# Kernel optimization log

Hardware: AMD Instinct MI355X
Metric: run time of the kernel (lower is better)

## Reference

```python
import jax, jax.numpy as jnp
import numpy as np

# DeepNovo config constants
MASS_H2O = 18.01056
MASS_NH3 = 17.02655
MS_RESOLUTION = 10.0          # bins per Dalton
WINDOW_SIZE = 10
MAX_MZ = 30000                # 3000 Da * 10 bins/Da
_PAD, _GO, _EOS = 0, 1, 2
VOCAB = 26
BATCH = 32768


def setup_inputs() -> dict:
    key = jax.random.key(0)
    k1, k2, k3, k4 = jax.random.split(key, 4)
    spectrum = jax.random.uniform(k1, (MAX_MZ,), dtype=jnp.float32)
    pepmass = jax.random.uniform(k2, (BATCH,), dtype=jnp.float32, minval=500.0, maxval=2500.0)
    prefix_mass = jax.random.uniform(k3, (BATCH,), dtype=jnp.float32) * pepmass * 0.8
    # amino-acid residue masses roughly in [57, 186] Da
    masses = jax.random.uniform(k4, (VOCAB,), dtype=jnp.float32, minval=57.0, maxval=186.0)
    return {"spectrum": spectrum, "pepmass": pepmass, "prefix_mass": prefix_mass,
            "masses": masses, "direction": 0}


def reference(spectrum, pepmass, prefix_mass, masses, direction):
    if direction == 0:
        first_label, last_label = _GO, _EOS
        cb = prefix_mass[:, None] + masses[None, :]      # [B, V]
        cy = pepmass[:, None] - cb
    else:
        first_label, last_label = _EOS, _GO
        cy = prefix_mass[:, None] + masses[None, :]
        cb = pepmass[:, None] - cy
    # 8 ion types: b, b-H2O, b-NH3, b++, y, y-H2O, y-NH3, y++  -> [B, V, 8]
    ion_mass = jnp.stack([cb, cb - MASS_H2O, cb - MASS_NH3, cb / 2,
                          cy, cy - MASS_H2O, cy - MASS_NH3, cy / 2], axis=-1)
    inf_idx = jnp.round(ion_mass * MS_RESOLUTION).astype(jnp.int32) - WINDOW_SIZE // 2
    valid = (inf_idx >= 0) & (inf_idx <= MAX_MZ - WINDOW_SIZE)   # [B, V, 8]
    safe = jnp.where(valid, inf_idx, 0)
    slices = safe[..., None] + jnp.arange(WINDOW_SIZE, dtype=jnp.int32)  # [B, V, 8, W]
    gathered = jnp.take(spectrum, slices) * valid[..., None].astype(spectrum.dtype)
    # zero out FIRST/LAST/PAD vocab rows (for both directions the set is {_PAD,_GO,_EOS})
    label_mask = jnp.ones((VOCAB,), spectrum.dtype).at[
        jnp.array([_PAD, first_label, last_label])].set(0.0)
    return gathered * label_mask[None, :, None, None]
```

## Files before the change

kernel.cpp:

```cpp
#include <hip/hip_runtime.h>
#include <hip/hip_fp16.h>


#define MASS_H2O 18.01056f
#define MASS_NH3 17.02655f

typedef float floatx4 __attribute__((ext_vector_type(4)));

constexpr int MAX_MZ = 30000;
constexpr int WIN = 10;
constexpr int CPR = 520;
constexpr int BLOCK = 960;
constexpr int GRID  = 494;
constexpr int THREADS = GRID * BLOCK;
constexpr int ROW_STEP = THREADS / CPR;
constexpr int KIT = 36;
constexpr int CHUNK = 18;
constexpr int KMAX = 37;
constexpr int DROWS = 3;
constexpr int SPAD = 30004;

__global__ __launch_bounds__(BLOCK) void intensity_kernel(
    const float* __restrict__ spectrum,
    const float* __restrict__ pepmass,
    const float* __restrict__ prefix_mass,
    const float* __restrict__ masses,
    const int*   __restrict__ dir_p,
    float* __restrict__ out,
    int batch)
{
    __shared__ __half  sspec[SPAD];
    __shared__ float2  spmf[DROWS * KMAX];

    const int tid  = (int)blockIdx.x * BLOCK + (int)threadIdx.x;
    const int blkR = ((int)blockIdx.x * BLOCK) / CPR;

    {
        const float2* sp2 = reinterpret_cast<const float2*>(spectrum);
        __half2* dst = reinterpret_cast<__half2*>(sspec);
#pragma unroll 4
        for (int i = threadIdx.x; i < MAX_MZ / 2; i += BLOCK) {
            float2 t = sp2[i];
            dst[i] = __floats2half2_rn(t.x, t.y);
        }
        if (threadIdx.x < (SPAD - MAX_MZ) / 2)
            dst[MAX_MZ / 2 + threadIdx.x] = __floats2half2_rn(0.f, 0.f);
    }
    {
        int i = threadIdx.x;
        if (i < DROWS * KMAX) {
            int d = i / KMAX;
            int k = i - d * KMAX;
            int r = blkR + d + k * ROW_STEP;
            float2 val = {0.0f, 0.0f};
            if (r < batch) { val.x = pepmass[r]; val.y = prefix_mass[r]; }
            spmf[i] = val;
        }
    }

    const int col  = tid % CPR;
    const int row0 = tid / CPR;
    const int doff = (row0 - blkR) * KMAX;
    const int v = col / 20;
    const int q = col - v * 20;
    const float ms = masses[v];
    const bool lmb = (v > 2);
    const int dir = dir_p[0];

    const int e0 = 4 * q;
    const int ionA = e0 / 10,       wp0 = e0 - ionA * 10;
    const int ionB = (e0 + 2) / 10, wp1 = (e0 + 2) - ionB * 10;
    const bool suA = ((ionA >= 4) ^ (dir != 0));
    const bool suB = ((ionB >= 4) ^ (dir != 0));
    const int  kA = ionA & 3, kB = ionB & 3;
    const float ajA = (kA == 1) ? -MASS_H2O : (kA == 2) ? -MASS_NH3 : 0.0f;
    const float ajB = (kB == 1) ? -MASS_H2O : (kB == 2) ? -MASS_NH3 : 0.0f;
    const float mjA = (kA == 3) ? 5.0f : 10.0f;
    const float mjB = (kB == 3) ? 5.0f : 10.0f;

    __syncthreads();

    const bool lastOk = (row0 + (KIT - 1) * ROW_STEP) < batch;
    floatx4* op = reinterpret_cast<floatx4*>(out) + tid;
    const uint32_t* spec32 = reinterpret_cast<const uint32_t*>(sspec);

    floatx4 vbuf[CHUNK];

    for (int ph = 0; ph < KIT / CHUNK; ++ph) {
        const int kbase = ph * CHUNK;

#pragma unroll
        for (int kk = 0; kk < CHUNK; ++kk) {
            const int k = kbase + kk;
            float2 pp = spmf[doff + k];
            float t = pp.y + ms;
            float u = pp.x - t;

            float baseA = suA ? u : t;
            float fA = (baseA + ajA) * mjA;
            int idxA = (int)rintf(fA) - (WIN / 2);
            bool vA = (unsigned)idxA <= (unsigned)(MAX_MZ - WIN);
            int safeA = vA ? idxA : 0;
            float okA = (vA && lmb) ? 1.0f : 0.0f;

            float baseB = suB ? u : t;
            float fB = (baseB + ajB) * mjB;
            int idxB = (int)rintf(fB) - (WIN / 2);
            bool vB = (unsigned)idxB <= (unsigned)(MAX_MZ - WIN);
            int safeB = vB ? idxB : 0;
            float okB = (vB && lmb) ? 1.0f : 0.0f;

            int h0 = safeA + wp0, h1 = safeB + wp1;
            int dw0 = h0 >> 1,    dw1 = h1 >> 1;
            uint32_t a0 = spec32[dw0], a1 = spec32[dw0 + 1];
            uint32_t b0 = spec32[dw1], b1 = spec32[dw1 + 1];
            uint32_t r0 = (uint32_t)(((((uint64_t)a1) << 32) | a0) >> ((h0 & 1) << 4));
            uint32_t r1 = (uint32_t)(((((uint64_t)b1) << 32) | b0) >> ((h1 & 1) << 4));
            __half2 hv0 = *reinterpret_cast<__half2*>(&r0);
            __half2 hv1 = *reinterpret_cast<__half2*>(&r1);

            floatx4 r;
            r.x = __low2float(hv0)  * okA;
            r.y = __high2float(hv0) * okA;
            r.z = __low2float(hv1)  * okB;
            r.w = __high2float(hv1) * okB;
            vbuf[kk] = r;
        }

#pragma unroll
        for (int kk = 0; kk < CHUNK; ++kk) {
            const int k = kbase + kk;
            if (k != KIT - 1 || lastOk)
                op[(size_t)k * (size_t)THREADS] = vbuf[kk];
        }
    }
}

extern "C" void kernel_launch(void* const* d_in, const int* in_sizes, int n_in,
                              void* d_out, int out_size, void* d_ws, size_t ws_size,
                              hipStream_t stream) {
    const float* spectrum    = (const float*)d_in[0];
    const float* pepmass     = (const float*)d_in[1];
    const float* prefix_mass = (const float*)d_in[2];
    const float* masses      = (const float*)d_in[3];
    const int*   direction   = (const int*)d_in[4];
    float* out = (float*)d_out;

    int batch = in_sizes[1];
    intensity_kernel<<<GRID, BLOCK, 0, stream>>>(
        spectrum, pepmass, prefix_mass, masses, direction, out, batch);
}
```

Baseline: 273.5 us.

## Assign each wave a contiguous output window with per-column flag table

Work is remapped so that each wave writes a contiguous span of output float4s, 64 lanes stepping through the span across 36 iterations, instead of each thread striding by the whole grid. Per-column constants (mass, ion selectors, window offsets, label mask) are precomputed into a shared-memory table with packed flags, and each iteration reads its column entry from that table. Block size rises to 1024, and the grid is sized from the batch, so fewer blocks each stage the spectrum into LDS. The trade is an extra LDS table read and flag decode per iteration, in exchange for more local write streams and less redundant spectrum staging.

```diff
diff --git a/kernel.cpp b/kernel.cpp
--- a/kernel.cpp
+++ b/kernel.cpp
@@ -10,15 +10,12 @@
 constexpr int MAX_MZ = 30000;
 constexpr int WIN = 10;
 constexpr int CPR = 520;
-constexpr int BLOCK = 960;
-constexpr int GRID  = 494;
-constexpr int THREADS = GRID * BLOCK;
-constexpr int ROW_STEP = THREADS / CPR;
+constexpr int BLOCK = 1024;
 constexpr int KIT = 36;
-constexpr int CHUNK = 18;
-constexpr int KMAX = 37;
-constexpr int DROWS = 3;
+constexpr int WAVE_WIN = KIT * 64;
+constexpr int BLK_WIN = (BLOCK / 64) * WAVE_WIN;
 constexpr int SPAD = 30004;
+constexpr int NROW = 73;
 
 __global__ __launch_bounds__(BLOCK) void intensity_kernel(
     const float* __restrict__ spectrum,
@@ -30,10 +27,12 @@
     int batch)
 {
     __shared__ __half  sspec[SPAD];
-    __shared__ float2  spmf[DROWS * KMAX];
+    __shared__ uint2   stbl[CPR];
+    __shared__ float2  spmf[NROW];
 
-    const int tid  = (int)blockIdx.x * BLOCK + (int)threadIdx.x;
-    const int blkR = ((int)blockIdx.x * BLOCK) / CPR;
+    const unsigned fb      = (unsigned)blockIdx.x * (unsigned)BLK_WIN;
+    const unsigned totalF  = (unsigned)batch * (unsigned)CPR;
+    const unsigned rowBase = fb / (unsigned)CPR;
 
     {
         const float2* sp2 = reinterpret_cast<const float2*>(spectrum);
@@ -46,93 +45,100 @@
         if (threadIdx.x < (SPAD - MAX_MZ) / 2)
             dst[MAX_MZ / 2 + threadIdx.x] = __floats2half2_rn(0.f, 0.f);
     }
-    {
-        int i = threadIdx.x;
-        if (i < DROWS * KMAX) {
-            int d = i / KMAX;
-            int k = i - d * KMAX;
-            int r = blkR + d + k * ROW_STEP;
-            float2 val = {0.0f, 0.0f};
-            if (r < batch) { val.x = pepmass[r]; val.y = prefix_mass[r]; }
-            spmf[i] = val;
-        }
+    if (threadIdx.x < NROW) {
+        int r = (int)rowBase + (int)threadIdx.x;
+        float2 val = {0.0f, 0.0f};
+        if (r < batch) { val.x = pepmass[r]; val.y = prefix_mass[r]; }
+        spmf[threadIdx.x] = val;
     }
-
-    const int col  = tid % CPR;
-    const int row0 = tid / CPR;
-    const int doff = (row0 - blkR) * KMAX;
-    const int v = col / 20;
-    const int q = col - v * 20;
-    const float ms = masses[v];
-    const bool lmb = (v > 2);
-    const int dir = dir_p[0];
-
-    const int e0 = 4 * q;
-    const int ionA = e0 / 10,       wp0 = e0 - ionA * 10;
-    const int ionB = (e0 + 2) / 10, wp1 = (e0 + 2) - ionB * 10;
-    const bool suA = ((ionA >= 4) ^ (dir != 0));
-    const bool suB = ((ionB >= 4) ^ (dir != 0));
-    const int  kA = ionA & 3, kB = ionB & 3;
-    const float ajA = (kA == 1) ? -MASS_H2O : (kA == 2) ? -MASS_NH3 : 0.0f;
-    const float ajB = (kB == 1) ? -MASS_H2O : (kB == 2) ? -MASS_NH3 : 0.0f;
-    const float mjA = (kA == 3) ? 5.0f : 10.0f;
-    const float mjB = (kB == 3) ? 5.0f : 10.0f;
-
+    if (threadIdx.x < CPR) {
+        const int c = threadIdx.x;
+        const int dir = dir_p[0];
+        int v = c / 20, q = c - 20 * v;
+        int e0 = 4 * q;
+        int ionA = e0 / 10,       wp0 = e0 - 10 * ionA;
+        int ionB = (e0 + 2) / 10, wp1 = (e0 + 2) - 10 * ionB;
+        int kA = ionA & 3, kB = ionB & 3;
+        unsigned fl = (unsigned)wp0 | ((unsigned)wp1 << 4);
+        if ((ionA >= 4) ^ (dir != 0)) fl |= 1u << 8;
+        if ((ionB >= 4) ^ (dir != 0)) fl |= 1u << 9;
+        if (kA == 3) fl |= 1u << 10;
+        if (kB == 3) fl |= 1u << 11;
+        if (v > 2)   fl |= 1u << 12;
+        if (kA == 1) fl |= 1u << 16;
+        if (kA == 2) fl |= 1u << 17;
+        if (kB == 1) fl |= 1u << 18;
+        if (kB == 2) fl |= 1u << 19;
+        uint2 e;
+        e.x = __float_as_uint(masses[v]);
+        e.y = fl;
+        stbl[c] = e;
+    }
     __syncthreads();
 
-    const bool lastOk = (row0 + (KIT - 1) * ROW_STEP) < batch;
-    floatx4* op = reinterpret_cast<floatx4*>(out) + tid;
+    const int wv   = (int)threadIdx.x >> 6;
+    const int lane = (int)threadIdx.x & 63;
+    unsigned f   = fb + (unsigned)wv * (unsigned)WAVE_WIN + (unsigned)lane;
+    unsigned row = f / (unsigned)CPR;
+    unsigned col = f - row * (unsigned)CPR;
+    unsigned rel = row - rowBase;
+
     const uint32_t* spec32 = reinterpret_cast<const uint32_t*>(sspec);
+    floatx4* out4 = reinterpret_cast<floatx4*>(out);
 
-    floatx4 vbuf[CHUNK];
+#pragma unroll 4
+    for (int k = 0; k < KIT; ++k) {
+        float2 pp = spmf[rel];
+        uint2  tb = stbl[col];
+        float  ms = __uint_as_float(tb.x);
+        unsigned fl = tb.y;
+        float t = pp.y + ms;
+        float u = pp.x - t;
 
-    for (int ph = 0; ph < KIT / CHUNK; ++ph) {
-        const int kbase = ph * CHUNK;
+        float baseA = (fl & (1u << 8)) ? u : t;
+        float ajA = (fl & (1u << 16)) ? -MASS_H2O
+                  : (fl & (1u << 17)) ? -MASS_NH3 : 0.0f;
+        float mjA = (fl & (1u << 10)) ? 5.0f : 10.0f;
+        float fA = (baseA + ajA) * mjA;
+        int idxA = (int)rintf(fA) - (WIN / 2);
+        bool vA = (unsigned)idxA <= (unsigned)(MAX_MZ - WIN);
+        int safeA = vA ? idxA : 0;
+        float baseB = (fl & (1u << 9)) ? u : t;
+        float ajB = (fl & (1u << 18)) ? -MASS_H2O
+                  : (fl & (1u << 19)) ? -MASS_NH3 : 0.0f;
+        float mjB = (fl & (1u << 11)) ? 5.0f : 10.0f;
+        float fB = (baseB + ajB) * mjB;
+        int idxB = (int)rintf(fB) - (WIN / 2);
+        bool vB = (unsigned)idxB <= (unsigned)(MAX_MZ - WIN);
+        int safeB = vB ? idxB : 0;
 
-#pragma unroll
-        for (int kk = 0; kk < CHUNK; ++kk) {
-            const int k = kbase + kk;
-            float2 pp = spmf[doff + k];
-            float t = pp.y + ms;
-            float u = pp.x - t;
+        bool lmb = (fl & (1u << 12)) != 0;
+        float okA = (vA && lmb) ? 1.0f : 0.0f;
+        float okB = (vB && lmb) ? 1.0f : 0.0f;
 
-            float baseA = suA ? u : t;
-            float fA = (baseA + ajA) * mjA;
-            int idxA = (int)rintf(fA) - (WIN / 2);
-            bool vA = (unsigned)idxA <= (unsigned)(MAX_MZ - WIN);
-            int safeA = vA ? idxA : 0;
-            float okA = (vA && lmb) ? 1.0f : 0.0f;
+        int h0 = safeA + (int)(fl & 15u);
+        int h1 = safeB + (int)((fl >> 4) & 15u);
+        int dw0 = h0 >> 1, dw1 = h1 >> 1;
+        uint32_t a0 = spec32[dw0], a1 = spec32[dw0 + 1];
+        uint32_t b0 = spec32[dw1], b1 = spec32[dw1 + 1];
+        uint32_t r0 = (uint32_t)(((((uint64_t)a1) << 32) | a0) >> ((h0 & 1) << 4));
+        uint32_t r1 = (uint32_t)(((((uint64_t)b1) << 32) | b0) >> ((h1 & 1) << 4));
+        __half2 hv0 = *reinterpret_cast<__half2*>(&r0);
+        __half2 hv1 = *reinterpret_cast<__half2*>(&r1);
 
-            float baseB = suB ? u : t;
-            float fB = (baseB + ajB) * mjB;
-            int idxB = (int)rintf(fB) - (WIN / 2);
-            bool vB = (unsigned)idxB <= (unsigned)(MAX_MZ - WIN);
-            int safeB = vB ? idxB : 0;
-            float okB = (vB && lmb) ? 1.0f : 0.0f;
+        floatx4 r;
+        r.x = __low2float(hv0)  * okA;
+        r.y = __high2float(hv0) * okA;
+        r.z = __low2float(hv1)  * okB;
+        r.w = __high2float(hv1) * okB;
+        if (f < totalF)
+            out4[(size_t)f] = r;
 
-            int h0 = safeA + wp0, h1 = safeB + wp1;
-            int dw0 = h0 >> 1,    dw1 = h1 >> 1;
-            uint32_t a0 = spec32[dw0], a1 = spec32[dw0 + 1];
-            uint32_t b0 = spec32[dw1], b1 = spec32[dw1 + 1];
-            uint32_t r0 = (uint32_t)(((((uint64_t)a1) << 32) | a0) >> ((h0 & 1) << 4));
-            uint32_t r1 = (uint32_t)(((((uint64_t)b1) << 32) | b0) >> ((h1 & 1) << 4));
-            __half2 hv0 = *reinterpret_cast<__half2*>(&r0);
-            __half2 hv1 = *reinterpret_cast<__half2*>(&r1);
-
-            floatx4 r;
-            r.x = __low2float(hv0)  * okA;
-            r.y = __high2float(hv0) * okA;
-            r.z = __low2float(hv1)  * okB;
-            r.w = __high2float(hv1) * okB;
-            vbuf[kk] = r;
-        }
-
-#pragma unroll
-        for (int kk = 0; kk < CHUNK; ++kk) {
-            const int k = kbase + kk;
-            if (k != KIT - 1 || lastOk)
-                op[(size_t)k * (size_t)THREADS] = vbuf[kk];
-        }
+        f += 64u;
+        unsigned nc = col + 64u;
+        unsigned wrap = (nc >= (unsigned)CPR) ? 1u : 0u;
+        col = nc - wrap * (unsigned)CPR;
+        rel += wrap;
     }
 }
 
@@ -147,6 +153,8 @@
     float* out = (float*)d_out;
 
     int batch = in_sizes[1];
-    intensity_kernel<<<GRID, BLOCK, 0, stream>>>(
+    long long totalF = (long long)batch * CPR;
+    int grid = (int)((totalF + BLK_WIN - 1) / BLK_WIN);
+    intensity_kernel<<<grid, BLOCK, 0, stream>>>(
         spectrum, pepmass, prefix_mass, masses, direction, out, batch);
 }
```

Result: no change. 275.0 us (+0.5%).
